# Kernel optimization log

Measured on AMD Instinct MI355X. Metric: run time of the kernel, lower is better.

The kernel has to match this reference:

```python
import jax, jax.numpy as jnp
import numpy as np

H = 12  # num_heads

def _alibi_bias(num_heads, n, dtype):
    # slopes: ratio**i for i in 1..H, ratio = 2**(-8/H)
    ratio = 2.0 ** (-8.0 / num_heads)
    slopes = ratio ** jnp.arange(1, num_heads + 1, dtype=jnp.float32)  # [H]
    pos = jnp.arange(n)
    rel = jnp.abs(pos[None, :] - pos[:, None]).astype(jnp.float32)  # [N,N]
    return (-slopes[:, None, None] * rel[None]).astype(dtype)  # [H,N,N]

def setup_inputs() -> dict:
    key = jax.random.key(0)
    ks = jax.random.split(key, 5)
    B, N, C = 16, 1024, 768
    s = 0.02
    return {
        "x": jax.random.normal(ks[0], (B, N, C), jnp.float32),
        "w_qkv": jax.random.normal(ks[1], (3 * C, C), jnp.float32) * s,
        "b_qkv": jax.random.normal(ks[2], (3 * C,), jnp.float32) * s,
        "w_proj": jax.random.normal(ks[3], (C, C), jnp.float32) * s,
        "b_proj": jax.random.normal(ks[4], (C,), jnp.float32) * s,
    }

def reference(x, w_qkv, b_qkv, w_proj, b_proj):
    B, N, C = x.shape
    D = C // H
    scale = D ** -0.5
    qkv = x @ w_qkv.T + b_qkv                       # [B,N,3C]
    qkv = qkv.reshape(B, N, 3, H, D)
    q = qkv[:, :, 0].transpose(0, 2, 1, 3)          # [B,H,N,D]
    k = qkv[:, :, 1].transpose(0, 2, 1, 3)
    v = qkv[:, :, 2].transpose(0, 2, 1, 3)
    bias = _alibi_bias(H, N, x.dtype)               # [H,N,N]
    scores = jnp.einsum('bhnd,bhmd->bhnm', q, k) * scale + bias[None]
    attn = jax.nn.softmax(scores, axis=-1)
    out = jnp.einsum('bhnm,bhmd->bhnd', attn, v)    # [B,H,N,D]
    out = out.transpose(0, 2, 1, 3).reshape(B, N, C)
    return out @ w_proj.T + b_proj
```

## Files before the change

### kernel.cpp

```cpp
#include <hip/hip_runtime.h>


typedef unsigned short u16;
typedef unsigned int u32;
typedef __attribute__((ext_vector_type(8))) short short8;
typedef __attribute__((ext_vector_type(4))) float f32x4;

__device__ __forceinline__ u16 f2bf(float f) {
    u32 u = __float_as_uint(f);
    u32 r = u + 0x7FFFu + ((u >> 16) & 1u);
    return (u16)(r >> 16);
}

__device__ __forceinline__ f32x4 mfma16(short8 a, short8 b, f32x4 c) {
    return __builtin_amdgcn_mfma_f32_16x16x32_bf16(a, b, c, 0, 0, 0);
}
__device__ __forceinline__ u32 cvtpk_bf16(float lo, float hi) {
    u32 r;
    asm("v_cvt_pk_bf16_f32 %0, %1, %2" : "=v"(r) : "v"(lo), "v"(hi));
    return r;
}

__global__ void cvt_f32_bf16(const float* __restrict__ src, u16* __restrict__ dst, int n4) {
    int i = blockIdx.x * blockDim.x + threadIdx.x;
    int stride = gridDim.x * blockDim.x;
    for (int idx = i; idx < n4; idx += stride) {
        float4 v = *(const float4*)(src + (size_t)idx * 4);
        ushort4 o;
        o.x = f2bf(v.x); o.y = f2bf(v.y); o.z = f2bf(v.z); o.w = f2bf(v.w);
        *(ushort4*)(dst + (size_t)idx * 4) = o;
    }
}

template <int EPI>
__global__ __launch_bounds__(256) void gemm_nt(
    const u16* __restrict__ A, const u16* __restrict__ Bw,
    const float* __restrict__ bias, u16* __restrict__ outb, float* __restrict__ outf,
    int nTilesN)
{
    constexpr int K = 768;
    constexpr int LDK = 40;
    __shared__ __align__(16) u16 lA[2][128 * LDK];
    __shared__ __align__(16) u16 lB[2][128 * LDK];

    int tid = threadIdx.x;
    int bid = blockIdx.x;
    int nwg = gridDim.x;
    int cpx = nwg >> 3;
    int swz = (bid & 7) * cpx + (bid >> 3);
    int bm = swz / nTilesN;
    int bn = swz - bm * nTilesN;
    int m0 = bm * 128, n0 = bn * 128;

    int sr = tid >> 2;
    int sc = (tid & 3) << 3;
    const u16* pA = A + (size_t)(m0 + sr) * K + sc;
    const u16* pB = Bw + (size_t)(n0 + sr) * K + sc;

    uint4 ra0 = *(const uint4*)(pA);
    uint4 ra1 = *(const uint4*)(pA + (size_t)64 * K);
    uint4 rb0 = *(const uint4*)(pB);
    uint4 rb1 = *(const uint4*)(pB + (size_t)64 * K);

    int w = tid >> 6, lane = tid & 63;
    int wr = (w >> 1) << 6, wc = (w & 1) << 6;
    int fq = lane >> 4, fr = lane & 15;
    f32x4 acc[4][4] = {};

    int aoff = sr * LDK + sc;
    constexpr int nkt = K / 32;

    *(uint4*)&lA[0][aoff] = ra0; *(uint4*)&lA[0][aoff + 64 * LDK] = ra1;
    *(uint4*)&lB[0][aoff] = rb0; *(uint4*)&lB[0][aoff + 64 * LDK] = rb1;

    for (int kt = 0; kt < nkt; ++kt) {
        int cur = kt & 1;
        __syncthreads();
        if (kt + 1 < nkt) {
            const u16* qA = pA + (kt + 1) * 32;
            const u16* qB = pB + (kt + 1) * 32;
            ra0 = *(const uint4*)(qA);
            ra1 = *(const uint4*)(qA + (size_t)64 * K);
            rb0 = *(const uint4*)(qB);
            rb1 = *(const uint4*)(qB + (size_t)64 * K);
        }
        short8 af[4], bfr[4];
#pragma unroll
        for (int i = 0; i < 4; ++i)
            af[i] = *(const short8*)&lA[cur][(wr + i * 16 + fr) * LDK + fq * 8];
#pragma unroll
        for (int j = 0; j < 4; ++j)
            bfr[j] = *(const short8*)&lB[cur][(wc + j * 16 + fr) * LDK + fq * 8];
        __builtin_amdgcn_s_setprio(1);
#pragma unroll
        for (int i = 0; i < 4; ++i)
#pragma unroll
            for (int j = 0; j < 4; ++j)
                acc[i][j] = mfma16(af[i], bfr[j], acc[i][j]);
        __builtin_amdgcn_s_setprio(0);
        if (kt + 1 < nkt) {
            int nxt = cur ^ 1;
            *(uint4*)&lA[nxt][aoff] = ra0; *(uint4*)&lA[nxt][aoff + 64 * LDK] = ra1;
            *(uint4*)&lB[nxt][aoff] = rb0; *(uint4*)&lB[nxt][aoff + 64 * LDK] = rb1;
        }
    }

    if (EPI == 0) {
        int nbase = n0 + wc;
        int s = nbase / 768;
        int hh = (nbase % 768) >> 6;
        int b = m0 >> 10;
        int i0 = (m0 & 1023) + wr;
        u16* obase = outb + (((size_t)s * 16 + b) * 12 + hh) * 1024 * 64;
#pragma unroll
        for (int j = 0; j < 4; ++j) {
            float bval = bias[nbase + j * 16 + fr];
            int d = j * 16 + fr;
#pragma unroll
            for (int i = 0; i < 4; ++i) {
                int r0 = i0 + i * 16 + fq * 4;
#pragma unroll
                for (int r = 0; r < 4; ++r)
                    obase[(size_t)(r0 + r) * 64 + d] = f2bf(acc[i][j][r] + bval);
            }
        }
    } else {
#pragma unroll
        for (int j = 0; j < 4; ++j) {
            int col = n0 + wc + j * 16 + fr;
            float bval = bias[col];
#pragma unroll
            for (int i = 0; i < 4; ++i) {
                int row0 = m0 + wr + i * 16 + fq * 4;
#pragma unroll
                for (int r = 0; r < 4; ++r)
                    outf[(size_t)(row0 + r) * 768 + col] = acc[i][j][r] + bval;
            }
        }
    }
}

__global__ __launch_bounds__(256) void attn_alibi(
    const u16* __restrict__ QKV, u16* __restrict__ att)
{
    int bid = blockIdx.x;
    int qt = bid & 15;
    int bh = bid >> 4;
    int h = bh % 12;
    int b = bh / 12;
    int q0 = qt * 64;
    const u16* Qg = QKV + (size_t)bh * 65536;
    const u16* Kg = QKV + (size_t)(192 + bh) * 65536;
    const u16* Vg = QKV + (size_t)(384 + bh) * 65536;

    __shared__ __align__(16) u16 Qs[64][72];
    __shared__ __align__(16) u16 Ks[64][72];
    __shared__ __align__(16) u16 Vt[64][72];
    __shared__ __align__(16) u16 Ps[64][72];

    int tid = threadIdx.x, w = tid >> 6, lane = tid & 63;
    int fq = lane >> 4, fr = lane & 15;

    for (int c = tid; c < 512; c += 256) {
        int r = c >> 3, d = (c & 7) * 8;
        *(uint4*)&Qs[r][d] = *(const uint4*)(Qg + (size_t)(q0 + r) * 64 + d);
    }
    __syncthreads();
    short8 aq0 = *(const short8*)&Qs[w * 16 + fr][fq * 8];
    short8 aq1 = *(const short8*)&Qs[w * 16 + fr][32 + fq * 8];

    const float C1 = 0.125f * 1.44269504f;
    float c2 = __builtin_amdgcn_exp2f(-(2.0f / 3.0f) * (float)(h + 1)) * 1.44269504f;
    int distThr = (int)(40.0f / c2);
    int lo_kv = q0 - 63 - distThr;
    int hi_kv = q0 + 63 + distThr;
    int t_lo = (lo_kv <= 0) ? 0 : (lo_kv >> 6);
    int t_hi = (hi_kv >= 1023) ? 15 : (hi_kv >> 6);

    float di = (float)(q0 + w * 16 + fr - fq * 4);
    float lsum = 0.f;
    f32x4 acc[4] = {};

    for (int it = t_lo; it <= t_hi; ++it) {
        int kv0 = it * 64;
        __syncthreads();
        for (int c = tid; c < 512; c += 256) {
            int r = c >> 3, d = (c & 7) * 8;
            *(uint4*)&Ks[r][d] = *(const uint4*)(Kg + (size_t)(kv0 + r) * 64 + d);
            uint4 vv = *(const uint4*)(Vg + (size_t)(kv0 + r) * 64 + d);
            u16* vp = (u16*)&vv;
            int vs = r ^ ((c & 7) << 3);
#pragma unroll
            for (int jj = 0; jj < 8; ++jj) Vt[d + jj][vs] = vp[jj];
        }
        __syncthreads();

        f32x4 sfr[4];
        __builtin_amdgcn_s_setprio(1);
#pragma unroll
        for (int ct = 0; ct < 4; ++ct) {
            short8 bk0 = *(const short8*)&Ks[ct * 16 + fr][fq * 8];
            short8 bk1 = *(const short8*)&Ks[ct * 16 + fr][32 + fq * 8];
            f32x4 s0 = {0.f, 0.f, 0.f, 0.f};
            s0 = mfma16(bk0, aq0, s0);
            s0 = mfma16(bk1, aq1, s0);
            sfr[ct] = s0;
        }
        __builtin_amdgcn_s_setprio(0);

        float dkv = di - (float)kv0;
#pragma unroll
        for (int ct = 0; ct < 4; ++ct) {
#pragma unroll
            for (int rp = 0; rp < 2; ++rp) {
                float t0 = dkv - (float)(ct * 16 + rp * 2);
                float e0 = __builtin_amdgcn_exp2f(fmaf(sfr[ct][rp * 2], C1, -c2 * fabsf(t0)));
                float e1 = __builtin_amdgcn_exp2f(fmaf(sfr[ct][rp * 2 + 1], C1, -c2 * fabsf(t0 - 1.0f)));
                lsum += e0 + e1;
                *(u32*)&Ps[w * 16 + fr][ct * 16 + fq * 4 + rp * 2] = cvtpk_bf16(e0, e1);
            }
        }

        short8 pa0 = *(const short8*)&Ps[w * 16 + fr][fq * 8];
        short8 pa1 = *(const short8*)&Ps[w * 16 + fr][32 + fq * 8];
        __builtin_amdgcn_s_setprio(1);
#pragma unroll
        for (int dt = 0; dt < 4; ++dt) {
            int row = dt * 16 + fr;
            int swzr = (row >> 3) << 3;
            short8 bv0 = *(const short8*)&Vt[row][(fq * 8) ^ swzr];
            short8 bv1 = *(const short8*)&Vt[row][(32 + fq * 8) ^ swzr];
            acc[dt] = mfma16(pa0, bv0, acc[dt]);
            acc[dt] = mfma16(pa1, bv1, acc[dt]);
        }
        __builtin_amdgcn_s_setprio(0);
    }

    float l = lsum;
    l += __shfl_xor(l, 16);
    l += __shfl_xor(l, 32);
    float rlo = 1.0f / l;
    float rl[4];
#pragma unroll
    for (int r = 0; r < 4; ++r)
        rl[r] = __shfl(rlo, fq * 4 + r);

#pragma unroll
    for (int dt = 0; dt < 4; ++dt)
#pragma unroll
        for (int r = 0; r < 4; ++r) {
            int ig = q0 + w * 16 + fq * 4 + r;
            att[((size_t)(b * 1024 + ig) * 12 + h) * 64 + dt * 16 + fr] =
                (u16)cvtpk_bf16(acc[dt][r] * rl[r], 0.f);
        }
}

extern "C" void kernel_launch(void* const* d_in, const int* in_sizes, int n_in,
                              void* d_out, int out_size, void* d_ws, size_t ws_size,
                              hipStream_t stream) {
    const float* x      = (const float*)d_in[0];
    const float* w_qkv  = (const float*)d_in[1];
    const float* b_qkv  = (const float*)d_in[2];
    const float* w_proj = (const float*)d_in[3];
    const float* b_proj = (const float*)d_in[4];
    float* out = (float*)d_out;

    char* ws = (char*)d_ws;
    u16* Xb     = (u16*)ws;
    u16* Wqkvb  = (u16*)(ws + 25165824);
    u16* Wprojb = (u16*)(ws + 28704768);
    u16* QKVb   = (u16*)(ws + 29884416);
    u16* Attb   = Xb;

    cvt_f32_bf16<<<2048, 256, 0, stream>>>(x, Xb, 12582912 / 4);
    cvt_f32_bf16<<<1728, 256, 0, stream>>>(w_qkv, Wqkvb, 1769472 / 4);
    cvt_f32_bf16<<<576, 256, 0, stream>>>(w_proj, Wprojb, 589824 / 4);

    gemm_nt<0><<<128 * 18, 256, 0, stream>>>(Xb, Wqkvb, b_qkv, QKVb, nullptr, 18);
    attn_alibi<<<16 * 12 * 16, 256, 0, stream>>>(QKVb, Attb);
    gemm_nt<1><<<128 * 6, 256, 0, stream>>>(Attb, Wprojb, b_proj, nullptr, out, 6);
}
```

Before: 231.0 us.

## Prefetch next K/V tile into registers and remap attention blocks per XCD

The attention kernel now loads the next K/V tile from global memory into registers while the current tile is being computed, so load latency overlaps with MFMA and exp work instead of stalling each iteration. It also remaps block indices so each of the 8 XCDs handles a contiguous group of 24 batch-heads, which keeps all query tiles of a head on one XCD's L2 and improves K/V reuse. The register prefetch raises register pressure and could lower occupancy. The grid size of 3072 is unchanged.

```diff
diff --git a/kernel.cpp b/kernel.cpp
--- a/kernel.cpp
+++ b/kernel.cpp
@@ -143,9 +143,11 @@
 __global__ __launch_bounds__(256) void attn_alibi(
     const u16* __restrict__ QKV, u16* __restrict__ att)
 {
-    int bid = blockIdx.x;
-    int qt = bid & 15;
-    int bh = bid >> 4;
+    int g = blockIdx.x;
+    int xcd = g & 7;
+    int idx = g >> 3;
+    int qt = idx & 15;
+    int bh = xcd * 24 + (idx >> 4);
     int h = bh % 12;
     int b = bh / 12;
     int q0 = qt * 64;
@@ -177,23 +179,42 @@
     int t_lo = (lo_kv <= 0) ? 0 : (lo_kv >> 6);
     int t_hi = (hi_kv >= 1023) ? 15 : (hi_kv >> 6);
 
+    int sr0 = tid >> 3;
+    int sr1 = sr0 + 32;
+    int sc = (tid & 7) * 8;
+    int vswz = (tid & 7) << 3;
+
+    uint4 kr0 = *(const uint4*)(Kg + (size_t)(t_lo * 64 + sr0) * 64 + sc);
+    uint4 kr1 = *(const uint4*)(Kg + (size_t)(t_lo * 64 + sr1) * 64 + sc);
+    uint4 vr0 = *(const uint4*)(Vg + (size_t)(t_lo * 64 + sr0) * 64 + sc);
+    uint4 vr1 = *(const uint4*)(Vg + (size_t)(t_lo * 64 + sr1) * 64 + sc);
+
     float di = (float)(q0 + w * 16 + fr - fq * 4);
     float lsum = 0.f;
     f32x4 acc[4] = {};
 
     for (int it = t_lo; it <= t_hi; ++it) {
-        int kv0 = it * 64;
         __syncthreads();
-        for (int c = tid; c < 512; c += 256) {
-            int r = c >> 3, d = (c & 7) * 8;
-            *(uint4*)&Ks[r][d] = *(const uint4*)(Kg + (size_t)(kv0 + r) * 64 + d);
-            uint4 vv = *(const uint4*)(Vg + (size_t)(kv0 + r) * 64 + d);
-            u16* vp = (u16*)&vv;
-            int vs = r ^ ((c & 7) << 3);
-#pragma unroll
-            for (int jj = 0; jj < 8; ++jj) Vt[d + jj][vs] = vp[jj];
+        *(uint4*)&Ks[sr0][sc] = kr0;
+        *(uint4*)&Ks[sr1][sc] = kr1;
+        {
+            const u16* v0 = (const u16*)&vr0;
+            const u16* v1 = (const u16*)&vr1;
+#pragma unroll
+            for (int jj = 0; jj < 8; ++jj) {
+                Vt[sc + jj][sr0 ^ vswz] = v0[jj];
+                Vt[sc + jj][sr1 ^ vswz] = v1[jj];
+            }
         }
         __syncthreads();
+
+        if (it < t_hi) {
+            int kvn = (it + 1) * 64;
+            kr0 = *(const uint4*)(Kg + (size_t)(kvn + sr0) * 64 + sc);
+            kr1 = *(const uint4*)(Kg + (size_t)(kvn + sr1) * 64 + sc);
+            vr0 = *(const uint4*)(Vg + (size_t)(kvn + sr0) * 64 + sc);
+            vr1 = *(const uint4*)(Vg + (size_t)(kvn + sr1) * 64 + sc);
+        }
 
         f32x4 sfr[4];
         __builtin_amdgcn_s_setprio(1);
@@ -208,7 +229,7 @@
         }
         __builtin_amdgcn_s_setprio(0);
 
-        float dkv = di - (float)kv0;
+        float dkv = di - (float)(it * 64);
 #pragma unroll
         for (int ct = 0; ct < 4; ++ct) {
 #pragma unroll
@@ -277,6 +298,6 @@
     cvt_f32_bf16<<<576, 256, 0, stream>>>(w_proj, Wprojb, 589824 / 4);
 
     gemm_nt<0><<<128 * 18, 256, 0, stream>>>(Xb, Wqkvb, b_qkv, QKVb, nullptr, 18);
-    attn_alibi<<<16 * 12 * 16, 256, 0, stream>>>(QKVb, Attb);
+    attn_alibi<<<3072, 256, 0, stream>>>(QKVb, Attb);
     gemm_nt<1><<<128 * 6, 256, 0, stream>>>(Attb, Wprojb, b_proj, nullptr, out, 6);
 }
```

Result: faster. 216.1 us (-6.5%).
